# Kernel optimization log

Hardware: AMD Instinct MI355X
Metric: run time of the kernel (lower is better)

Reference implementation:

```python
import jax, jax.numpy as jnp
import numpy as np

NUM_STATION = 20
NUM_HEADS = 8
INPUT_DIM = 128
KEY_DIM = 16          # = val_dim = embed_dim // num_heads
EMBED_DIM = 128
NORM = 1.0 / np.sqrt(KEY_DIM).astype(np.float32)


def setup_inputs() -> dict:
    key = jax.random.key(0)
    ks = jax.random.split(key, 10)
    B, N, D = 32, 1024, INPUT_DIM
    q = jax.random.normal(ks[0], (B, N, D), jnp.float32)
    h = jax.random.normal(ks[1], (B, N, D), jnp.float32)
    stdv_k = 1.0 / np.sqrt(KEY_DIM)      # torch init: uniform(-1/sqrt(last_dim), ...)
    stdv_e = 1.0 / np.sqrt(EMBED_DIM)
    def U(k, shape, s):
        return jax.random.uniform(k, shape, jnp.float32, -s, s)
    pshape = (NUM_HEADS, INPUT_DIM, KEY_DIM)
    return {
        "q": q,
        "h": h,
        "W_query_custom": U(ks[2], pshape, stdv_k),
        "W_query_custom_1": U(ks[3], pshape, stdv_k),
        "W_key_custom": U(ks[4], pshape, stdv_k),
        "W_val_custom": U(ks[5], pshape, stdv_k),
        "W_query_charge_1": U(ks[6], pshape, stdv_k),
        "W_key_charge": U(ks[7], pshape, stdv_k),
        "W_val_charge": U(ks[8], pshape, stdv_k),
        "W_out": U(ks[9], (NUM_HEADS, KEY_DIM, EMBED_DIM), stdv_e),
    }


def reference(q, h, W_query_custom, W_query_custom_1, W_key_custom, W_val_custom,
              W_query_charge_1, W_key_charge, W_val_charge, W_out):
    S = NUM_STATION + 1                      # depot + stations
    h_st, h_tk = h[:, :S], h[:, S:]          # [B,S,D], [B,T,D]
    q_st, q_tk = q[:, :S], q[:, S:]

    proj = lambda x, W: jnp.einsum('bnd,hdk->hbnk', x, W)

    K_c = proj(h_tk, W_key_custom)           # [H,B,T,K]
    V_c = proj(h_tk, W_val_custom)
    K_s = proj(h_st, W_key_charge)           # [H,B,S,K]
    V_s = proj(h_st, W_val_charge)

    # task -> task attention (queries via W_query_custom_1)
    Q_tt = proj(q_tk, W_query_custom_1)
    A_tt = jax.nn.softmax(NORM * jnp.einsum('hbqk,hbtk->hbqt', Q_tt, K_c), axis=-1)
    heads_t = jnp.einsum('hbqt,hbtk->hbqk', A_tt, V_c)

    # task -> station attention (queries via W_query_custom)
    Q_ts = proj(q_tk, W_query_custom)
    A_ts = jax.nn.softmax(NORM * jnp.einsum('hbqk,hbsk->hbqs', Q_ts, K_s), axis=-1)
    heads_t = heads_t + jnp.einsum('hbqs,hbsk->hbqk', A_ts, V_s)

    # station -> task attention (queries via W_query_charge_1)
    Q_st = proj(q_st, W_query_charge_1)
    A_st = jax.nn.softmax(NORM * jnp.einsum('hbqk,hbtk->hbqt', Q_st, K_c), axis=-1)
    heads_s = jnp.einsum('hbqt,hbtk->hbqk', A_st, V_c)

    heads = jnp.concatenate([heads_s, heads_t], axis=2)   # [H,B,N,K]
    out = jnp.einsum('hbnk,hke->bne', heads, W_out)        # [B,N,E]
    return out
```

## Files before the change

kernel.cpp:

```cpp
#include <hip/hip_runtime.h>

typedef __bf16 bf16x8 __attribute__((ext_vector_type(8)));
typedef float f32x4 __attribute__((ext_vector_type(4)));
typedef float f32x16 __attribute__((ext_vector_type(16)));
typedef unsigned int uint32;
typedef unsigned short u16;

#define NST 21
#define TOK 1003
#define SCL 0.3606737602222409f

union U4B { uint4 u; bf16x8 b; };

__device__ __forceinline__ uint32 pkbf(float a, float b) {
  uint32 ua = __float_as_uint(a), ub = __float_as_uint(b);
  ua += 0x7fffu + ((ua >> 16) & 1u);
  ub += 0x7fffu + ((ub >> 16) & 1u);
  return (ua >> 16) | (ub & 0xffff0000u);
}
__device__ __forceinline__ u16 bf1(float a) {
  uint32 u = __float_as_uint(a);
  u += 0x7fffu + ((u >> 16) & 1u);
  return (u16)(u >> 16);
}
__device__ __forceinline__ uint32 pkperm(float lo, float hi) {
  return __builtin_amdgcn_perm(__float_as_uint(hi), __float_as_uint(lo), 0x07060302u);
}
__device__ __forceinline__ void plswap(uint32& a, uint32& b) {
#if __has_builtin(__builtin_amdgcn_permlane32_swap)
  typedef unsigned int uu2 __attribute__((ext_vector_type(2)));
  uu2 r = __builtin_amdgcn_permlane32_swap(a, b, false, false);
  a = r.x; b = r.y;
#else
  asm volatile("v_permlane32_swap_b32 %0, %1" : "+v"(a), "+v"(b));
#endif
}

__global__ __launch_bounds__(256) void prep(
    const float* __restrict__ q, const float* __restrict__ hx,
    const float* __restrict__ W0, const float* __restrict__ W1,
    const float* __restrict__ W2, const float* __restrict__ W3,
    const float* __restrict__ W4, const float* __restrict__ Wqst,
    const float* __restrict__ Wks, const float* __restrict__ Wvs,
    u16* __restrict__ WtAll, u16* __restrict__ Qm,
    u16* __restrict__ Ks, u16* __restrict__ Vs) {
  int bid = blockIdx.x, tid = threadIdx.x;
  __shared__ float xq2[2][128], xh2[2][128];
  if (bid < 40) {
    int w = bid >> 3, seg = bid & 7;
    const float* W = (w == 0) ? W0 : (w == 1) ? W1 : (w == 2) ? W2
                     : (w == 3) ? W3 : W4;
    u16* dst = WtAll + w * 16384;
#pragma unroll
    for (int it = 0; it < 8; ++it) {
      int i = seg * 2048 + it * 256 + tid;
      int inner = i & 127, outer = i >> 7;
      float v;
      if (w < 4) {
        int h = outer >> 4, k = outer & 15;
        v = W[h * 2048 + inner * 16 + k];
      } else {
        v = W[inner * 128 + outer];
      }
      dst[outer * 128 + inner] = bf1(v);
    }
  } else {
    int t2 = bid - 40;
    int sub = tid >> 7, col = tid & 127;
    int hh = col >> 4, k = col & 15;
    int bs2 = t2 * 2 + sub;
    int b2 = bs2 >> 5, s = bs2 & 31;
    if (s < NST) {
      xq2[sub][col] = q[(size_t)(b2 * 1024 + s) * 128 + col];
      xh2[sub][col] = hx[(size_t)(b2 * 1024 + s) * 128 + col];
    }
    __syncthreads();
    if (s < NST) {
      const float* Wq = Wqst + hh * 2048 + k;
      const float* Wk = Wks + hh * 2048 + k;
      const float* Wv = Wvs + hh * 2048 + k;
      float dq = 0.f, dk_ = 0.f, dv = 0.f;
#pragma unroll 8
      for (int d = 0; d < 128; ++d) {
        float xq = xq2[sub][d], xh = xh2[sub][d];
        dq = fmaf(xq, Wq[d * 16], dq);
        dk_ = fmaf(xh, Wk[d * 16], dk_);
        dv = fmaf(xh, Wv[d * 16], dv);
      }
      Qm[(((size_t)hh * 32 + b2) * 1024 + s) * 16 + k] = bf1(dq * SCL);
      Ks[(((size_t)hh * 32 + b2) * 32 + s) * 16 + k] = bf1(dk_);
      Vs[(((size_t)hh * 32 + b2) * 16 + k) * 32 + s] = bf1(dv);
    } else {
      Ks[(((size_t)hh * 32 + b2) * 32 + s) * 16 + k] = 0;
      Vs[(((size_t)hh * 32 + b2) * 16 + k) * 32 + s] = 0;
    }
  }
}

__global__ __launch_bounds__(256) void proj_pair(
    const float* __restrict__ q, const float* __restrict__ hx,
    const u16* __restrict__ WtAll, u16* __restrict__ Qm,
    u16* __restrict__ Qts, u16* __restrict__ Kc, u16* __restrict__ Vc) {
  __shared__ u16 Wl[128 * 136];
  int pg = blockIdx.x >> 9, mb = blockIdx.x & 511;
  int m0 = mb * 64;
  const float* A = pg ? hx : q;
  int tid = threadIdx.x;
  int wave = tid >> 6, lane = tid & 63;
  int quad = lane >> 4, l15 = lane & 15;
  int mrow = m0 + wave * 16 + l15;

  U4B af[4];
#pragma unroll
  for (int dk = 0; dk < 4; ++dk) {
    const float* Af = A + (size_t)mrow * 128 + dk * 32 + quad * 8;
    float4 a = *(const float4*)Af;
    float4 b = *(const float4*)(Af + 4);
    af[dk].u = make_uint4(pkbf(a.x, a.y), pkbf(a.z, a.w),
                          pkbf(b.x, b.y), pkbf(b.z, b.w));
  }

  int gbase = m0 + wave * 16 + quad * 4;
  int bb = gbase >> 10, n0 = gbase & 1023;
  int token = mrow;
  int bb2 = token >> 10, tn = token & 1023;

#pragma unroll
  for (int s = 0; s < 2; ++s) {
    int mode = pg * 2 + s;
    const u16* WtG = WtAll + mode * 16384;
    if (s) __syncthreads();
#pragma unroll
    for (int r = 0; r < 8; ++r) {
      int i = r * 256 + tid;
      int e = i >> 4, j = i & 15;
      *(uint4*)&Wl[e * 136 + j * 8] = *(const uint4*)(WtG + e * 128 + j * 8);
    }
    __syncthreads();

    f32x4 c[8];
#pragma unroll
    for (int nt = 0; nt < 8; ++nt)
#pragma unroll
      for (int r = 0; r < 4; ++r) c[nt][r] = 0.f;
#pragma unroll
    for (int dk = 0; dk < 4; ++dk)
#pragma unroll
      for (int nt = 0; nt < 8; ++nt) {
        U4B bg;
        bg.u = *(const uint4*)&Wl[(nt * 16 + l15) * 136 + dk * 32 + quad * 8];
        if (mode == 3)
          c[nt] = __builtin_amdgcn_mfma_f32_16x16x32_bf16(af[dk].b, bg.b, c[nt], 0, 0, 0);
        else
          c[nt] = __builtin_amdgcn_mfma_f32_16x16x32_bf16(bg.b, af[dk].b, c[nt], 0, 0, 0);
      }

    if (mode == 3) {
#pragma unroll
      for (int nt = 0; nt < 8; ++nt) {
        uint2 w2 = make_uint2(pkbf(c[nt][0], c[nt][1]), pkbf(c[nt][2], c[nt][3]));
        *(uint2*)(Vc + (((size_t)nt * 32 + bb) * 16 + l15) * 1024 + n0) = w2;
      }
    } else {
      float scale = (mode <= 1) ? SCL : 1.0f;
      u16* dstp = (mode == 0) ? Qm : (mode == 1) ? Qts : Kc;
      if (mode != 0 || tn >= NST) {
#pragma unroll
        for (int nt = 0; nt < 8; ++nt) {
          uint2 w2 = make_uint2(pkbf(c[nt][0] * scale, c[nt][1] * scale),
                                pkbf(c[nt][2] * scale, c[nt][3] * scale));
          *(uint2*)(dstp + (((size_t)nt * 32 + bb2) * 1024 + tn) * 16 + quad * 4) = w2;
        }
      }
    }
  }
}

__global__ __launch_bounds__(256) void outproj(
    const u16* __restrict__ heads, const u16* __restrict__ WtAll,
    float* __restrict__ out) {
  __shared__ u16 Wl[128 * 136];
  const u16* WtG = WtAll + 4 * 16384;
  int tid = threadIdx.x;
#pragma unroll
  for (int r = 0; r < 8; ++r) {
    int i = r * 256 + tid;
    int e = i >> 4, j = i & 15;
    *(uint4*)&Wl[e * 136 + j * 8] = *(const uint4*)(WtG + e * 128 + j * 8);
  }
  __syncthreads();
  int wave = tid >> 6, lane = tid & 63;
  int quad = lane >> 4, l15 = lane & 15;
  int m0 = blockIdx.x * 64;
  int mrow = m0 + wave * 16 + l15;

  f32x4 c[8];
#pragma unroll
  for (int nt = 0; nt < 8; ++nt)
#pragma unroll
    for (int r = 0; r < 4; ++r) c[nt][r] = 0.f;
#pragma unroll
  for (int dk = 0; dk < 4; ++dk) {
    U4B af;
    int h2 = dk * 2 + (quad >> 1);
    int k0 = (quad & 1) * 8;
    af.u = *(const uint4*)(heads + ((size_t)h2 * 32768 + mrow) * 16 + k0);
#pragma unroll
    for (int nt = 0; nt < 8; ++nt) {
      U4B bg;
      bg.u = *(const uint4*)&Wl[(nt * 16 + l15) * 136 + dk * 32 + quad * 8];
      c[nt] = __builtin_amdgcn_mfma_f32_16x16x32_bf16(bg.b, af.b, c[nt], 0, 0, 0);
    }
  }
#pragma unroll
  for (int nt = 0; nt < 8; ++nt)
    *(f32x4*)(out + (size_t)mrow * 128 + nt * 16 + quad * 4) = c[nt];
}

__global__ __launch_bounds__(512, 4) void attn_main(
    const u16* __restrict__ Qm, const u16* __restrict__ Qts,
    const u16* __restrict__ Kc, const u16* __restrict__ Vc,
    const u16* __restrict__ Ks, const u16* __restrict__ Vs,
    u16* __restrict__ heads) {
  int bx = blockIdx.x;
  int hb = bx & 255, qc = bx >> 8;
  int h = hb >> 5, b = hb & 31;
  int tid = threadIdx.x;
  int wave = tid >> 6, lane = tid & 63;
  int l5 = lane >> 5, l31 = lane & 31;

  __shared__ u16 Kl[128 * 26];
  __shared__ u16 Vl[32 * 140];
  __shared__ u16 KsL[32 * 26];
  __shared__ u16 VsL[32 * 44];

  const u16* Qbase = Qm + ((size_t)(h * 32 + b)) * 16384;
  const u16* QtsB = Qts + ((size_t)(h * 32 + b)) * 16384;
  const u16* Kbase = Kc + ((size_t)(h * 32 + b)) * 16384;
  const u16* Vbase = Vc + ((size_t)(h * 32 + b)) * 16384;
  const u16* KsB = Ks + (size_t)(h * 32 + b) * 512;
  const u16* VsB = Vs + (size_t)(h * 32 + b) * 512;

  uint4 ones4 = make_uint4(0x3F803F80u, 0x3F803F80u, 0x3F803F80u, 0x3F803F80u);

  if (tid < 64) {
    int key = tid >> 1, half = tid & 1;
    *(uint4*)&KsL[key * 26 + half * 8] = *(const uint4*)(KsB + key * 16 + half * 8);
  } else if (tid < 128) {
    int t = tid - 64;
    int d = t >> 2, kg = t & 3;
    *(uint4*)&VsL[d * 44 + kg * 8] = *(const uint4*)(VsB + d * 32 + kg * 8);
  } else if (tid < 192) {
    int t = tid - 128;
    *(uint4*)&VsL[(16 + (t >> 2)) * 44 + (t & 3) * 8] = ones4;
  }
  if (tid < 256)
    *(uint4*)&Vl[(16 + (tid >> 4)) * 140 + (tid & 15) * 8] = ones4;

  int skey = tid >> 2, shalf = tid & 3;
  int sd = tid >> 5, skg = tid & 31;
  uint2 kpre = *(const uint2*)(Kbase + (size_t)skey * 16 + shalf * 4);
  uint2 vpre = *(const uint2*)(Vbase + (size_t)sd * 1024 + skg * 4);

  int qw0 = qc * 256 + wave * 32;
  int qrow = qw0 + l31;

  f32x16 zero16;
#pragma unroll
  for (int i = 0; i < 16; ++i) zero16[i] = 0.f;

  U4B qf;
  qf.u = *(const uint4*)(QtsB + (size_t)qrow * 16 + l5 * 8);
  __syncthreads();
  float contrib[8];
  {
    U4B af;
    af.u = *(const uint4*)&KsL[l31 * 26 + l5 * 8];
    f32x16 c0 =
        __builtin_amdgcn_mfma_f32_32x32x16_bf16(af.b, qf.b, zero16, 0, 0, 0);
    uint32 w[8];
#pragma unroll
    for (int g = 0; g < 4; ++g) {
      float p0 = __builtin_amdgcn_exp2f(c0[4 * g + 0]);
      float p1 = __builtin_amdgcn_exp2f(c0[4 * g + 1]);
      float p2 = __builtin_amdgcn_exp2f(c0[4 * g + 2]);
      float p3 = __builtin_amdgcn_exp2f(c0[4 * g + 3]);
      int kb0 = 8 * g + 4 * l5;
      p0 = (kb0 + 0 >= NST) ? 0.f : p0;
      p1 = (kb0 + 1 >= NST) ? 0.f : p1;
      p2 = (kb0 + 2 >= NST) ? 0.f : p2;
      p3 = (kb0 + 3 >= NST) ? 0.f : p3;
      w[2 * g] = pkperm(p0, p1);
      w[2 * g + 1] = pkperm(p2, p3);
    }
    plswap(w[0], w[2]); plswap(w[1], w[3]);
    plswap(w[4], w[6]); plswap(w[5], w[7]);
    U4B b1, b2, a1, a2;
    b1.u = make_uint4(w[0], w[1], w[2], w[3]);
    b2.u = make_uint4(w[4], w[5], w[6], w[7]);
    a1.u = *(const uint4*)&VsL[l31 * 44 + l5 * 8];
    a2.u = *(const uint4*)&VsL[l31 * 44 + 16 + l5 * 8];
    f32x16 acc2 =
        __builtin_amdgcn_mfma_f32_32x32x16_bf16(a1.b, b1.b, zero16, 0, 0, 0);
    acc2 = __builtin_amdgcn_mfma_f32_32x32x16_bf16(a2.b, b2.b, acc2, 0, 0, 0);
    float rla2 = __builtin_amdgcn_rcpf(acc2[8]);
#pragma unroll
    for (int r = 0; r < 8; ++r) contrib[r] = acc2[r] * rla2;
  }

  qf.u = *(const uint4*)(Qbase + (size_t)qrow * 16 + l5 * 8);
  f32x16 acc;
#pragma unroll
  for (int i = 0; i < 16; ++i) acc[i] = 0.f;

#pragma unroll 1
  for (int kb = 0; kb < 8; ++kb) {
    __syncthreads();
    *(uint2*)&Kl[skey * 26 + shalf * 4] = kpre;
    *(uint2*)&Vl[sd * 140 + skg * 4] = vpre;
    if (kb < 7) {
      int j0n = (kb + 1) * 128;
      kpre = *(const uint2*)(Kbase + (size_t)(j0n + skey) * 16 + shalf * 4);
      vpre = *(const uint2*)(Vbase + (size_t)sd * 1024 + j0n + skg * 4);
    }
    __syncthreads();

    U4B af0;
    af0.u = *(const uint4*)&Kl[l31 * 26 + l5 * 8];
    f32x16 c0 =
        __builtin_amdgcn_mfma_f32_32x32x16_bf16(af0.b, qf.b, zero16, 0, 0, 0);
#pragma unroll
    for (int kt = 0; kt < 4; ++kt) {
      f32x16 cn;
      if (kt < 3) {
        U4B afn;
        afn.u = *(const uint4*)&Kl[((kt + 1) * 32 + l31) * 26 + l5 * 8];
        cn = __builtin_amdgcn_mfma_f32_32x32x16_bf16(afn.b, qf.b, zero16, 0, 0, 0);
      }
      int key0 = kt * 32;
      bool masked = (kb == 0) && (kt == 0);
      uint32 w[8];
#pragma unroll
      for (int g = 0; g < 4; ++g) {
        float p0 = __builtin_amdgcn_exp2f(c0[4 * g + 0]);
        float p1 = __builtin_amdgcn_exp2f(c0[4 * g + 1]);
        float p2 = __builtin_amdgcn_exp2f(c0[4 * g + 2]);
        float p3 = __builtin_amdgcn_exp2f(c0[4 * g + 3]);
        if (masked) {
          int kb0 = 8 * g + 4 * l5;
          p0 = (kb0 + 0 < NST) ? 0.f : p0;
          p1 = (kb0 + 1 < NST) ? 0.f : p1;
          p2 = (kb0 + 2 < NST) ? 0.f : p2;
          p3 = (kb0 + 3 < NST) ? 0.f : p3;
        }
        w[2 * g] = pkperm(p0, p1);
        w[2 * g + 1] = pkperm(p2, p3);
      }
      plswap(w[0], w[2]); plswap(w[1], w[3]);
      plswap(w[4], w[6]); plswap(w[5], w[7]);
      U4B b1, b2, a1, a2;
      b1.u = make_uint4(w[0], w[1], w[2], w[3]);
      b2.u = make_uint4(w[4], w[5], w[6], w[7]);
      a1.u = *(const uint4*)&Vl[l31 * 140 + key0 + l5 * 8];
      a2.u = *(const uint4*)&Vl[l31 * 140 + key0 + 16 + l5 * 8];
      acc = __builtin_amdgcn_mfma_f32_32x32x16_bf16(a1.b, b1.b, acc, 0, 0, 0);
      acc = __builtin_amdgcn_mfma_f32_32x32x16_bf16(a2.b, b2.b, acc, 0, 0, 0);
      if (kt < 3) c0 = cn;
    }
  }

  {
    float rla = __builtin_amdgcn_rcpf(acc[8]);
    bool tok = (qrow >= NST);
    float v0 = acc[0] * rla + (tok ? contrib[0] : 0.f);
    float v1 = acc[1] * rla + (tok ? contrib[1] : 0.f);
    float v2 = acc[2] * rla + (tok ? contrib[2] : 0.f);
    float v3 = acc[3] * rla + (tok ? contrib[3] : 0.f);
    float v4 = acc[4] * rla + (tok ? contrib[4] : 0.f);
    float v5 = acc[5] * rla + (tok ? contrib[5] : 0.f);
    float v6 = acc[6] * rla + (tok ? contrib[6] : 0.f);
    float v7 = acc[7] * rla + (tok ? contrib[7] : 0.f);
    u16* hrow = heads + (((size_t)(h * 32 + b)) * 1024 + qrow) * 16;
    *(uint2*)(hrow + 4 * l5) = make_uint2(pkbf(v0, v1), pkbf(v2, v3));
    *(uint2*)(hrow + 8 + 4 * l5) = make_uint2(pkbf(v4, v5), pkbf(v6, v7));
  }
}

extern "C" void kernel_launch(void* const* d_in, const int* in_sizes, int n_in,
                              void* d_out, int out_size, void* d_ws,
                              size_t ws_size, hipStream_t stream) {
  (void)in_sizes; (void)n_in; (void)out_size; (void)ws_size;
  const float* q     = (const float*)d_in[0];
  const float* hx    = (const float*)d_in[1];
  const float* W_qts = (const float*)d_in[2];
  const float* W_qtt = (const float*)d_in[3];
  const float* W_kc  = (const float*)d_in[4];
  const float* W_vc  = (const float*)d_in[5];
  const float* W_qst = (const float*)d_in[6];
  const float* W_ks  = (const float*)d_in[7];
  const float* W_vs  = (const float*)d_in[8];
  const float* W_out = (const float*)d_in[9];

  char* ws = (char*)d_ws;
  u16* heads = (u16*)(ws + 0);
  u16* Qm    = (u16*)(ws + 16777216);
  u16* Qts   = (u16*)(ws + 25165824);
  u16* Kc    = (u16*)(ws + 33554432);
  u16* Vc    = (u16*)(ws + 41943040);
  u16* Ks    = (u16*)(ws + 50331648);
  u16* Vs    = (u16*)(ws + 50593792);
  u16* WtAll = (u16*)(ws + 50855936);

  hipLaunchKernelGGL(prep, dim3(552), dim3(256), 0, stream,
                     q, hx, W_qtt, W_qts, W_kc, W_vc, W_out, W_qst, W_ks, W_vs,
                     WtAll, Qm, Ks, Vs);
  hipLaunchKernelGGL(proj_pair, dim3(1024), dim3(256), 0, stream,
                     q, hx, WtAll, Qm, Qts, Kc, Vc);
  hipLaunchKernelGGL(attn_main, dim3(1024), dim3(512), 0, stream,
                     Qm, Qts, Kc, Vc, Ks, Vs, heads);
  hipLaunchKernelGGL(outproj, dim3(512), dim3(256), 0, stream,
                     heads, WtAll, (float*)d_out);
}
```

Measured before the change: 154.9 us.

## Double-buffer K/V tiles in shared memory to halve per-iteration barriers

```diff
diff --git a/kernel.cpp b/kernel.cpp
--- a/kernel.cpp
+++ b/kernel.cpp
@@ -229,8 +229,8 @@
   int wave = tid >> 6, lane = tid & 63;
   int l5 = lane >> 5, l31 = lane & 31;
 
-  __shared__ u16 Kl[128 * 26];
-  __shared__ u16 Vl[32 * 140];
+  __shared__ u16 Kl[2][128 * 26];
+  __shared__ u16 Vl[2][32 * 140];
   __shared__ u16 KsL[32 * 26];
   __shared__ u16 VsL[32 * 44];
 
@@ -254,8 +254,10 @@
     int t = tid - 128;
     *(uint4*)&VsL[(16 + (t >> 2)) * 44 + (t & 3) * 8] = ones4;
   }
-  if (tid < 256)
-    *(uint4*)&Vl[(16 + (tid >> 4)) * 140 + (tid & 15) * 8] = ones4;
+  {
+    int vb = tid >> 8, t = tid & 255;
+    *(uint4*)&Vl[vb][(16 + (t >> 4)) * 140 + (t & 15) * 8] = ones4;
+  }
 
   int skey = tid >> 2, shalf = tid & 3;
   int sd = tid >> 5, skg = tid & 31;
@@ -271,7 +273,14 @@
 
   U4B qf;
   qf.u = *(const uint4*)(QtsB + (size_t)qrow * 16 + l5 * 8);
+
+  *(uint2*)&Kl[0][skey * 26 + shalf * 4] = kpre;
+  *(uint2*)&Vl[0][sd * 140 + skg * 4] = vpre;
+  kpre = *(const uint2*)(Kbase + (size_t)(128 + skey) * 16 + shalf * 4);
+  vpre = *(const uint2*)(Vbase + (size_t)sd * 1024 + 128 + skg * 4);
+
   __syncthreads();
+
   float contrib[8];
   {
     U4B af;
@@ -315,18 +324,19 @@
 
 #pragma unroll 1
   for (int kb = 0; kb < 8; ++kb) {
-    __syncthreads();
-    *(uint2*)&Kl[skey * 26 + shalf * 4] = kpre;
-    *(uint2*)&Vl[sd * 140 + skg * 4] = vpre;
+    int cb = kb & 1;
     if (kb < 7) {
-      int j0n = (kb + 1) * 128;
-      kpre = *(const uint2*)(Kbase + (size_t)(j0n + skey) * 16 + shalf * 4);
-      vpre = *(const uint2*)(Vbase + (size_t)sd * 1024 + j0n + skg * 4);
-    }
-    __syncthreads();
+      *(uint2*)&Kl[cb ^ 1][skey * 26 + shalf * 4] = kpre;
+      *(uint2*)&Vl[cb ^ 1][sd * 140 + skg * 4] = vpre;
+      if (kb < 6) {
+        int j0n = (kb + 2) * 128;
+        kpre = *(const uint2*)(Kbase + (size_t)(j0n + skey) * 16 + shalf * 4);
+        vpre = *(const uint2*)(Vbase + (size_t)sd * 1024 + j0n + skg * 4);
+      }
+    }
 
     U4B af0;
-    af0.u = *(const uint4*)&Kl[l31 * 26 + l5 * 8];
+    af0.u = *(const uint4*)&Kl[cb][l31 * 26 + l5 * 8];
     f32x16 c0 =
         __builtin_amdgcn_mfma_f32_32x32x16_bf16(af0.b, qf.b, zero16, 0, 0, 0);
 #pragma unroll
@@ -334,7 +344,7 @@
       f32x16 cn;
       if (kt < 3) {
         U4B afn;
-        afn.u = *(const uint4*)&Kl[((kt + 1) * 32 + l31) * 26 + l5 * 8];
+        afn.u = *(const uint4*)&Kl[cb][((kt + 1) * 32 + l31) * 26 + l5 * 8];
         cn = __builtin_amdgcn_mfma_f32_32x32x16_bf16(afn.b, qf.b, zero16, 0, 0, 0);
       }
       int key0 = kt * 32;
@@ -361,12 +371,13 @@
       U4B b1, b2, a1, a2;
       b1.u = make_uint4(w[0], w[1], w[2], w[3]);
       b2.u = make_uint4(w[4], w[5], w[6], w[7]);
-      a1.u = *(const uint4*)&Vl[l31 * 140 + key0 + l5 * 8];
-      a2.u = *(const uint4*)&Vl[l31 * 140 + key0 + 16 + l5 * 8];
+      a1.u = *(const uint4*)&Vl[cb][l31 * 140 + key0 + l5 * 8];
+      a2.u = *(const uint4*)&Vl[cb][l31 * 140 + key0 + 16 + l5 * 8];
       acc = __builtin_amdgcn_mfma_f32_32x32x16_bf16(a1.b, b1.b, acc, 0, 0, 0);
       acc = __builtin_amdgcn_mfma_f32_32x32x16_bf16(a2.b, b2.b, acc, 0, 0, 0);
       if (kt < 3) c0 = cn;
     }
+    __syncthreads();
   }
 
   {
```

Result: no change. 153.8 us (-0.7%).
